# Kernel tuning notes

Measured on AMD Instinct MI355X. Metric: run time of the kernel, lower is better.

The kernel has to match this reference:

```python
import jax, jax.numpy as jnp
import numpy as np
from math import factorial

LMAX = 4
N_COEFF = (LMAX + 1) ** 2      # 25 real spherical-harmonic coefficients
N_RADII = 300                  # distance_bins
N_NODES = 512
FEAT = 128
RES_BETA, RES_ALPHA = 180, 360
DIST_STEP = 0.05


def _sh_basis(lmax, y, alpha):
    """Real spherical harmonics evaluated on a (beta, alpha) product grid.
    y = cos(beta) quadrature nodes. Returns [res_beta, res_alpha, (lmax+1)^2]."""
    B, A = len(y), len(alpha)
    P = np.zeros((lmax + 1, lmax + 1, B))
    P[0, 0] = 1.0
    s = np.sqrt(np.clip(1.0 - y * y, 0.0, None))
    for m in range(1, lmax + 1):
        P[m, m] = -(2 * m - 1) * s * P[m - 1, m - 1]
    for m in range(lmax):
        P[m + 1, m] = (2 * m + 1) * y * P[m, m]
    for m in range(lmax + 1):
        for l in range(m + 2, lmax + 1):
            P[l, m] = ((2 * l - 1) * y * P[l - 1, m] - (l + m - 1) * P[l - 2, m]) / (l - m)
    cols = []
    for l in range(lmax + 1):
        for m in range(-l, l + 1):
            am = abs(m)
            Nlm = np.sqrt((2 * l + 1) / (4 * np.pi) * factorial(l - am) / factorial(l + am))
            if m == 0:
                col = Nlm * P[l, 0][:, None] * np.ones((1, A))
            elif m > 0:
                col = np.sqrt(2.0) * Nlm * P[l, m][:, None] * np.cos(m * alpha)[None, :]
            else:
                col = np.sqrt(2.0) * Nlm * P[l, am][:, None] * np.sin(am * alpha)[None, :]
            cols.append(col)
    return np.stack(cols, axis=-1).astype(np.float32)


def setup_inputs() -> dict:
    key = jax.random.key(0)
    ks = jax.random.split(key, 14)

    def lin(k, a, b):
        return jax.random.normal(k, (a, b), jnp.float32) / np.float32(np.sqrt(a))

    x = jax.random.normal(ks[0], (N_NODES, FEAT), jnp.float32)
    fd = [FEAT, 128, 128, 64, 16, 2]
    td = [FEAT, 128, 128, 128, 128, 128, 6]
    fW = [lin(ks[1 + i], fd[i], fd[i + 1]) for i in range(5)]
    tW = [lin(ks[6 + i], td[i], td[i + 1]) for i in range(6)]
    pos_w = lin(ks[12], 2 * FEAT, N_RADII * N_COEFF)
    type_emb = jax.random.normal(ks[13], (5, FEAT), jnp.float32)

    y_np, w_np = np.polynomial.legendre.leggauss(RES_BETA)
    alpha_np = np.linspace(0.0, 2.0 * np.pi, RES_ALPHA, endpoint=False)
    basis = jnp.asarray(_sh_basis(LMAX, y_np, alpha_np))          # [B, A, C]
    qw = jnp.asarray(w_np / 2.0, jnp.float32)                     # gausslegendre / 2
    y_grid = jnp.asarray(y_np, jnp.float32)
    alpha_grid = jnp.asarray(alpha_np, jnp.float32)

    return {
        "x": x,
        "focus_w1": fW[0], "focus_w2": fW[1], "focus_w3": fW[2], "focus_w4": fW[3], "focus_w5": fW[4],
        "type_w1": tW[0], "type_w2": tW[1], "type_w3": tW[2], "type_w4": tW[3], "type_w5": tW[4], "type_w6": tW[5],
        "pos_w": pos_w, "type_emb": type_emb,
        "basis": basis, "qw": qw, "y_grid": y_grid, "alpha_grid": alpha_grid,
        "res_beta": RES_BETA, "res_alpha": RES_ALPHA,
    }


def reference(x, focus_w1, focus_w2, focus_w3, focus_w4, focus_w5,
              type_w1, type_w2, type_w3, type_w4, type_w5, type_w6,
              pos_w, type_emb, basis, qw, y_grid, alpha_grid,
              res_beta, res_alpha):
    n_nodes = x.shape[0]

    # --- focus MLP (relu), per-node logits; STOP logit 0 appended ---
    h = x
    for W in (focus_w1, focus_w2, focus_w3, focus_w4):
        h = jax.nn.relu(h @ W)
    focus_scores = (h @ focus_w5)[:, 0]                             # [n_nodes]
    focus_probs = jax.nn.softmax(jnp.concatenate([focus_scores, jnp.zeros((1,), x.dtype)]))
    focus = jnp.minimum(jnp.argmax(focus_probs), n_nodes - 1)

    # --- type MLP (softplus) on the focus node's features ---
    feat_f = x[focus]                                               # [128]
    th = feat_f
    for W in (type_w1, type_w2, type_w3, type_w4, type_w5):
        th = jax.nn.softplus(th @ W)
    type_dist = jax.nn.softmax(th @ type_w6)                        # [6]
    type_idx = jnp.minimum(jnp.argmax(type_dist), 4)

    # --- position head: SH coefficients per radial shell ---
    pos_in = jnp.concatenate([feat_f, type_emb[type_idx]])          # [256]
    coeffs = (pos_in @ pos_w).reshape(N_RADII, N_COEFF)             # [R, C]

    # to_s2grid: log-density on the sphere for every radial shell
    f = jnp.einsum('rc,bac->rba', coeffs, basis)                    # [R, B, A]
    log_meas = jnp.log(qw)[:, None] + jnp.log(2.0 * jnp.pi / res_alpha)  # [B, 1]

    # radial distribution: integral of exp(f) over the sphere, per shell
    log_radial = jax.nn.logsumexp(f + log_meas[None], axis=(1, 2))  # [R]
    radial_probs = jax.nn.softmax(log_radial)

    key = jax.random.key(42)
    k_r, k_a = jax.random.split(key)
    r_idx = jax.random.categorical(k_r, log_radial)

    # angular distribution at the sampled radius, normalized on S2
    fr = f[r_idx]                                                   # [B, A]
    logZr = jax.nn.logsumexp(fr + log_meas)
    angular_dist = jnp.exp(fr - logZr)                              # [B, A]

    joint_log = (fr + log_meas - logZr).reshape(-1)
    idx = jax.random.categorical(k_a, joint_log)
    y_i = idx // res_alpha
    a_i = idx % res_alpha

    radius_pred = (r_idx.astype(jnp.float32) + 1.0) * DIST_STEP
    return (type_dist, radial_probs, angular_dist, radius_pred, y_grid[y_i], alpha_grid[a_i])
```

## Files before the change

kernel.cpp:

```cpp
#include <hip/hip_runtime.h>
#include <math.h>
#include <stdint.h>

#define NNODES 512
#define FEAT   128
#define NR     300
#define NC     25
#define NB     180
#define NA     360
#define RSPLIT 4
#define BCHUNK (NB / RSPLIT)
#define O_TYPE   0
#define O_RAD    6
#define O_ANG    306
#define O_RADIUS 65106
#define O_Y      65107
#define O_ALPHA  65108

#define WS_KEYS   0
#define WS_FOCUS  4
#define WS_TYPEI  5
#define WS_RIDX   6
#define WS_INVZ   7
#define WS_DEAD   8
#define WS_SCORES 320
#define WS_POSIN  832
#define WS_PSUM   1088
#define WS_PV     1280
#define WS_PI     1472
#define WS_Q      1664
#define WS_HR     6176
#define WS_COEF   8352
#define WS_LRP    15872

#define GB_MLP   NNODES
#define GB_PREP  36
#define GB_PFT   162
#define GB_PFP   768
#define GB_TOTAL (GB_MLP + GB_PREP + GB_PFT + GB_PFP)

__constant__ int c_m_of_c[25] = {0,-1,0,1,-2,-1,0,1,2,-3,-2,-1,0,1,2,3,-4,-3,-2,-1,0,1,2,3,4};
__constant__ int c_h_cnt[9] = {5,4,3,2,1,4,3,2,1};
__constant__ int c_h_idx[9][5] = {
  {0,2,6,12,20},
  {3,7,13,21,0},
  {8,14,22,0,0},
  {15,23,0,0,0},
  {24,0,0,0,0},
  {1,5,11,19,0},
  {4,10,18,0,0},
  {9,17,0,0,0},
  {16,0,0,0,0}};

__device__ __forceinline__ void tf2x32(uint32_t k0, uint32_t k1, uint32_t x0, uint32_t x1,
                                       uint32_t& o0, uint32_t& o1) {
  uint32_t ks2 = k0 ^ k1 ^ 0x1BD11BDAu;
#define TF_RND(r) { x0 += x1; x1 = (x1 << r) | (x1 >> (32 - r)); x1 ^= x0; }
  x0 += k0; x1 += k1;
  TF_RND(13) TF_RND(15) TF_RND(26) TF_RND(6)
  x0 += k1; x1 += ks2 + 1u;
  TF_RND(17) TF_RND(29) TF_RND(16) TF_RND(24)
  x0 += ks2; x1 += k0 + 2u;
  TF_RND(13) TF_RND(15) TF_RND(26) TF_RND(6)
  x0 += k0; x1 += k1 + 3u;
  TF_RND(17) TF_RND(29) TF_RND(16) TF_RND(24)
  x0 += k1; x1 += ks2 + 4u;
  TF_RND(13) TF_RND(15) TF_RND(26) TF_RND(6)
  x0 += ks2; x1 += k0 + 5u;
#undef TF_RND
  o0 = x0; o1 = x1;
}

__device__ __forceinline__ float gumbel32(uint32_t k0, uint32_t k1, uint32_t lo) {
  uint32_t o0, o1; tf2x32(k0, k1, 0u, lo, o0, o1);
  uint32_t bits = o0 ^ o1;
  float u = __uint_as_float((bits >> 9) | 0x3f800000u) - 1.0f;
  u = fmaxf(u, 1.1754944e-38f);
  return -logf(-logf(u));
}

__global__ __launch_bounds__(128) void k_front(const float* __restrict__ x,
    const float* __restrict__ w1, const float* __restrict__ w2, const float* __restrict__ w3,
    const float* __restrict__ w4, const float* __restrict__ w5,
    const float* __restrict__ basis, const float* __restrict__ alpha_grid,
    const float* __restrict__ tw1, const float* __restrict__ tw2, const float* __restrict__ tw3,
    const float* __restrict__ tw4, const float* __restrict__ tw5, const float* __restrict__ tw6,
    const float* __restrict__ pos_w,
    float* __restrict__ wsf) {
  int bx = blockIdx.x;
  if (bx >= GB_MLP + GB_PREP + GB_PFT) {
    int pb = bx - (GB_MLP + GB_PREP + GB_PFT);
    const float4* p4 = (const float4*)pos_w;
    const int n4 = NR * NC * 256 / 4;
    float acc = 0.f;
    for (int i = pb * 128 + threadIdx.x; i < n4; i += GB_PFP * 128) {
      float4 v = p4[i];
      acc += v.x + v.y + v.z + v.w;
    }
    if (acc == -1.2345678e30f) wsf[WS_DEAD] = acc;
    return;
  }
  if (bx >= GB_MLP + GB_PREP) {
    int pb = bx - (GB_MLP + GB_PREP);
    int base = pb * 128;
    float acc = 0.f;
    int i = base + threadIdx.x;
    const float4* mats[5] = {(const float4*)tw1, (const float4*)tw2, (const float4*)tw3,
                             (const float4*)tw4, (const float4*)tw5};
    int mi = pb >> 5;
    if (mi < 5) {
      int li = (pb & 31) * 128 + threadIdx.x;
      float4 v = mats[mi][li];
      acc += v.x + v.y + v.z + v.w;
    } else {
      int li = (pb - 160) * 128 + threadIdx.x;
      if (li < 192) { float4 v = ((const float4*)tw6)[li]; acc += v.x + v.y + v.z + v.w; }
    }
    (void)i;
    if (acc == -1.2345678e30f) wsf[WS_DEAD] = acc;
    return;
  }
  if (bx >= GB_MLP) {
    int t = (bx - GB_MLP) * 128 + threadIdx.x;
    if (bx == GB_MLP && threadIdx.x == 0) {
      uint32_t* wu = (uint32_t*)wsf;
      uint32_t o0, o1;
      tf2x32(0u, 42u, 0u, 0u, o0, o1); wu[WS_KEYS + 0] = o0; wu[WS_KEYS + 1] = o1;
      tf2x32(0u, 42u, 0u, 1u, o0, o1); wu[WS_KEYS + 2] = o0; wu[WS_KEYS + 3] = o1;
    }
    if (t < NB * NC) {
      int b = t / NC, c = t % NC;
      int m = c_m_of_c[c];
      float q;
      if (m >= 0) {
        q = basis[(b * NA + 0) * NC + c];
      } else {
        float a10 = alpha_grid[10];
        q = basis[(b * NA + 10) * NC + c] / sinf((float)(-m) * a10);
      }
      wsf[WS_Q + t] = q;
    }
    return;
  }
  __shared__ float ha[128], hb[128];
  int n = bx, j = threadIdx.x;
  ha[j] = x[n * FEAT + j];
  __syncthreads();
  float acc = 0.f;
#pragma unroll 8
  for (int k = 0; k < 128; k++) acc += ha[k] * w1[k * 128 + j];
  hb[j] = fmaxf(acc, 0.f);
  __syncthreads();
  acc = 0.f;
#pragma unroll 8
  for (int k = 0; k < 128; k++) acc += hb[k] * w2[k * 128 + j];
  ha[j] = fmaxf(acc, 0.f);
  __syncthreads();
  if (j < 64) {
    acc = 0.f;
#pragma unroll 8
    for (int k = 0; k < 128; k++) acc += ha[k] * w3[k * 64 + j];
    hb[j] = fmaxf(acc, 0.f);
  }
  __syncthreads();
  if (j < 16) {
    acc = 0.f;
#pragma unroll
    for (int k = 0; k < 64; k++) acc += hb[k] * w4[k * 16 + j];
    ha[j] = fmaxf(acc, 0.f);
  }
  __syncthreads();
  if (j == 0) {
    acc = 0.f;
#pragma unroll
    for (int k = 0; k < 16; k++) acc += ha[k] * w5[k * 2 + 0];
    wsf[WS_SCORES + n] = acc;
  }
}

__global__ __launch_bounds__(1024) void k_type(const float* __restrict__ x,
    const float* __restrict__ w1, const float* __restrict__ w2, const float* __restrict__ w3,
    const float* __restrict__ w4, const float* __restrict__ w5, const float* __restrict__ w6,
    const float* __restrict__ type_emb, float* __restrict__ out, float* __restrict__ wsf) {
  __shared__ float src[128];
  __shared__ float partial[8][128];
  __shared__ float wrv[16]; __shared__ int wri[16];
  __shared__ float lg[6];
  __shared__ int f_sh, ti_sh;
  int t = threadIdx.x;
  int lane = t & 63, wid = t >> 6;
  float bv = -INFINITY; int bi = 1 << 30;
  if (t < NNODES + 1) { bv = (t < NNODES) ? wsf[WS_SCORES + t] : 0.f; bi = t; }
  for (int off = 32; off; off >>= 1) {
    float v2 = __shfl_down(bv, off); int i2 = __shfl_down(bi, off);
    if (v2 > bv || (v2 == bv && i2 < bi)) { bv = v2; bi = i2; }
  }
  if (lane == 0) { wrv[wid] = bv; wri[wid] = bi; }
  __syncthreads();
  if (t == 0) {
    float v0 = wrv[0]; int i0 = wri[0];
    for (int w = 1; w < 16; w++)
      if (wrv[w] > v0 || (wrv[w] == v0 && wri[w] < i0)) { v0 = wrv[w]; i0 = wri[w]; }
    int focus = (i0 < NNODES - 1) ? i0 : (NNODES - 1);
    ((int*)wsf)[WS_FOCUS] = focus;
    f_sh = focus;
  }
  __syncthreads();
  int focus = f_sh;
  if (t < 128) { float xv = x[focus * FEAT + t]; src[t] = xv; wsf[WS_POSIN + t] = xv; }
  __syncthreads();
  const float* Ws[5] = {w1, w2, w3, w4, w5};
#pragma unroll
  for (int L = 0; L < 5; L++) {
    const float* W = Ws[L];
    int j = t & 127, kc = t >> 7;
    float acc = 0.f;
#pragma unroll
    for (int k = 0; k < 16; k++) acc += src[kc * 16 + k] * W[(kc * 16 + k) * 128 + j];
    partial[kc][j] = acc;
    __syncthreads();
    if (t < 128) {
      float s = 0.f;
#pragma unroll
      for (int q = 0; q < 8; q++) s += partial[q][t];
      src[t] = fmaxf(s, 0.f) + log1pf(expf(-fabsf(s)));
    }
    __syncthreads();
  }
  float prod = 0.f;
  if (t < 768) { int o = t >> 7, j = t & 127; prod = src[j] * w6[j * 6 + o]; }
  for (int off = 32; off; off >>= 1) prod += __shfl_down(prod, off);
  if (t < 768 && lane == 0) wrv[wid] = prod;
  __syncthreads();
  if (t == 0) {
    for (int o = 0; o < 6; o++) lg[o] = wrv[2 * o] + wrv[2 * o + 1];
    float M = lg[0]; int am = 0;
    for (int i = 1; i < 6; i++) if (lg[i] > M) { M = lg[i]; am = i; }
    float e[6], S = 0.f;
    for (int i = 0; i < 6; i++) { e[i] = expf(lg[i] - M); S += e[i]; }
    for (int i = 0; i < 6; i++) out[O_TYPE + i] = e[i] / S;
    int ti = (am < 4) ? am : 4;
    ((int*)wsf)[WS_TYPEI] = ti;
    ti_sh = ti;
  }
  __syncthreads();
  if (t < 128) wsf[WS_POSIN + 128 + t] = type_emb[ti_sh * FEAT + t];
}

__global__ __launch_bounds__(256) void k_coeffs(const float* __restrict__ pos_w,
                                                float* __restrict__ wsf) {
  __shared__ float pin[256];
  __shared__ float partial[4][64];
  int t = threadIdx.x;
  pin[t] = wsf[WS_POSIN + t];
  __syncthreads();
  int oL = t & 63, kc = t >> 6;
  int o = blockIdx.x * 64 + oL;
  float acc = 0.f;
  if (o < NR * NC) {
#pragma unroll 16
    for (int k = 0; k < 64; k++) acc += pin[kc * 64 + k] * pos_w[(kc * 64 + k) * (NR * NC) + o];
  }
  partial[kc][oL] = acc;
  __syncthreads();
  if (kc == 0 && o < NR * NC)
    wsf[WS_COEF + o] = partial[0][oL] + partial[1][oL] + partial[2][oL] + partial[3][oL];
}

__global__ __launch_bounds__(384) void k_radial_lse(const float* __restrict__ qw,
    const float* __restrict__ alpha_grid, float* __restrict__ wsf) {
  __shared__ float4 Hs4[BCHUNK * 3];
  __shared__ float cs[NC];
  __shared__ float wred[6];
  int bx = blockIdx.x;
  int r = bx >> 2, s = bx & 3;
  int b0 = s * BCHUNK;
  int t = threadIdx.x;
  float* Hs = (float*)Hs4;
  if (t < NC) cs[t] = wsf[WS_COEF + r * NC + t];
  __syncthreads();
  const float LOGM = -4.0482054576f;
  for (int p = t; p < BCHUNK * 9; p += 384) {
    int b = p / 9, jj = p % 9;
    int bg = b0 + b;
    int n = c_h_cnt[jj];
    float acc = 0.f;
    for (int q = 0; q < n; q++) { int c = c_h_idx[jj][q]; acc += cs[c] * wsf[WS_Q + bg * NC + c]; }
    if (jj == 0) acc += logf(qw[bg]) + LOGM;
    Hs[b * 12 + jj] = acc;
  }
  __syncthreads();
  int a = t;
  float c1 = 0, c2 = 0, c3 = 0, c4 = 0, s1 = 0, s2 = 0, s3 = 0, s4 = 0;
  bool act = a < NA;
  if (act) {
    float al = alpha_grid[a];
    sincosf(al, &s1, &c1);
    sincosf(2.f * al, &s2, &c2);
    sincosf(3.f * al, &s3, &c3);
    sincosf(4.f * al, &s4, &c4);
  }
  float acc = 0.f;
#pragma unroll 5
  for (int b = 0; b < BCHUNK; b++) {
    float4 h0 = Hs4[b * 3 + 0], h1 = Hs4[b * 3 + 1], h2 = Hs4[b * 3 + 2];
    float f = h0.x + h0.y * c1 + h0.z * c2 + h0.w * c3 + h1.x * c4
            + h1.y * s1 + h1.z * s2 + h1.w * s3 + h2.x * s4;
    acc += act ? __expf(f) : 0.f;
  }
  for (int off = 32; off; off >>= 1) acc += __shfl_down(acc, off);
  int wid = t >> 6, lane = t & 63;
  if (lane == 0) wred[wid] = acc;
  __syncthreads();
  if (t == 0) {
    float ss = 0.f;
    for (int w = 0; w < 6; w++) ss += wred[w];
    wsf[WS_LRP + bx] = ss;
  }
}

__global__ __launch_bounds__(256) void k_radial_sample(float* __restrict__ out,
                                                       float* __restrict__ wsf) {
  __shared__ float ssh[NR], lrsh[NR];
  __shared__ float wr[4]; __shared__ int wi[4];
  __shared__ float Ssh; __shared__ int rsh;
  int t = threadIdx.x;
  const uint32_t* wu = (const uint32_t*)wsf;
  uint32_t kr0 = wu[WS_KEYS + 0], kr1 = wu[WS_KEYS + 1];
  for (int i = t; i < NR; i += 256) {
    float s = wsf[WS_LRP + i * 4] + wsf[WS_LRP + i * 4 + 1]
            + wsf[WS_LRP + i * 4 + 2] + wsf[WS_LRP + i * 4 + 3];
    ssh[i] = s;
    lrsh[i] = logf(s);
  }
  __syncthreads();
  float ss = 0.f;
  for (int i = t; i < NR; i += 256) ss += ssh[i];
  for (int off = 32; off; off >>= 1) ss += __shfl_down(ss, off);
  if ((t & 63) == 0) wr[t >> 6] = ss;
  __syncthreads();
  if (t == 0) Ssh = wr[0] + wr[1] + wr[2] + wr[3];
  __syncthreads();
  float S = Ssh;
  for (int i = t; i < NR; i += 256) out[O_RAD + i] = ssh[i] / S;
  float bv = -INFINITY; int bi = 1 << 30;
  for (int i = t; i < NR; i += 256) {
    float v = lrsh[i] + gumbel32(kr0, kr1, (uint32_t)i);
    if (v > bv || (v == bv && i < bi)) { bv = v; bi = i; }
  }
  for (int off = 32; off; off >>= 1) {
    float v2 = __shfl_down(bv, off); int i2 = __shfl_down(bi, off);
    if (v2 > bv || (v2 == bv && i2 < bi)) { bv = v2; bi = i2; }
  }
  if ((t & 63) == 0) { wr[t >> 6] = bv; wi[t >> 6] = bi; }
  __syncthreads();
  if (t == 0) {
    float v0 = wr[0]; int i0 = wi[0];
    for (int w = 1; w < 4; w++)
      if (wr[w] > v0 || (wr[w] == v0 && wi[w] < i0)) { v0 = wr[w]; i0 = wi[w]; }
    rsh = i0;
    ((int*)wsf)[WS_RIDX] = i0;
    out[O_RADIUS] = (float)(i0 + 1) * 0.05f;
  }
  __syncthreads();
  int r = rsh;
  for (int p = t; p < NB * 9; p += 256) {
    int b = p / 9, jj = p % 9, n = c_h_cnt[jj];
    float acc = 0.f;
    for (int q = 0; q < n; q++) {
      int c = c_h_idx[jj][q];
      acc += wsf[WS_COEF + r * NC + c] * wsf[WS_Q + b * NC + c];
    }
    wsf[WS_HR + b * 12 + jj] = acc;
  }
}

__global__ __launch_bounds__(384) void k_ang_partial(const float* __restrict__ qw,
    const float* __restrict__ alpha_grid, float* __restrict__ out, float* __restrict__ wsf) {
  __shared__ float wred[6]; __shared__ float wrv[6]; __shared__ int wri[6];
  int b = blockIdx.x, t = threadIdx.x;
  const uint32_t* wu = (const uint32_t*)wsf;
  uint32_t ka0 = wu[WS_KEYS + 2], ka1 = wu[WS_KEYS + 3];
  const float4* hr4 = (const float4*)(wsf + WS_HR + b * 12);
  float4 h0 = hr4[0], h1 = hr4[1], h2 = hr4[2];
  const float MEAS = 0.01745329252f;
  float elm = qw[b] * MEAS;
  float lm = logf(elm);
  float e = 0.f, v = -INFINITY; int idx = b * NA + t;
  if (t < NA) {
    float al = alpha_grid[t];
    float s1, c1, s2, c2, s3, c3, s4, c4;
    sincosf(al, &s1, &c1); sincosf(2.f * al, &s2, &c2);
    sincosf(3.f * al, &s3, &c3); sincosf(4.f * al, &s4, &c4);
    float f = h0.x + h0.y * c1 + h0.z * c2 + h0.w * c3 + h1.x * c4
            + h1.y * s1 + h1.z * s2 + h1.w * s3 + h2.x * s4;
    float ef = __expf(f);
    out[O_ANG + idx] = ef;
    e = ef * elm;
    v = f + lm + gumbel32(ka0, ka1, (uint32_t)idx);
  }
  int wid = t >> 6, lane = t & 63;
  for (int off = 32; off; off >>= 1) e += __shfl_down(e, off);
  if (lane == 0) wred[wid] = e;
  for (int off = 32; off; off >>= 1) {
    float v2 = __shfl_down(v, off); int i2 = __shfl_down(idx, off);
    if (v2 > v || (v2 == v && i2 < idx)) { v = v2; idx = i2; }
  }
  if (lane == 0) { wrv[wid] = v; wri[wid] = idx; }
  __syncthreads();
  if (t == 0) {
    float zs = 0.f;
    float v0 = wrv[0]; int i0 = wri[0];
    for (int w = 0; w < 6; w++) {
      zs += wred[w];
      if (w && (wrv[w] > v0 || (wrv[w] == v0 && wri[w] < i0))) { v0 = wrv[w]; i0 = wri[w]; }
    }
    wsf[WS_PSUM + b] = zs;
    wsf[WS_PV + b] = v0;
    ((int*)wsf)[WS_PI + b] = i0;
  }
}

__global__ __launch_bounds__(256) void k_ang_final(const float* __restrict__ y_grid,
    const float* __restrict__ alpha_grid, float* __restrict__ out, float* __restrict__ wsf) {
  __shared__ float wr[4]; __shared__ int wi[4];
  int t = threadIdx.x;
  float sv = (t < NB) ? wsf[WS_PSUM + t] : 0.f;
  for (int off = 32; off; off >>= 1) sv += __shfl_down(sv, off);
  if ((t & 63) == 0) wr[t >> 6] = sv;
  __syncthreads();
  if (t == 0) wsf[WS_INVZ] = 1.0f / (wr[0] + wr[1] + wr[2] + wr[3]);
  __syncthreads();
  float v = (t < NB) ? wsf[WS_PV + t] : -INFINITY;
  int i = (t < NB) ? ((const int*)wsf)[WS_PI + t] : (1 << 30);
  for (int off = 32; off; off >>= 1) {
    float v2 = __shfl_down(v, off); int i2 = __shfl_down(i, off);
    if (v2 > v || (v2 == v && i2 < i)) { v = v2; i = i2; }
  }
  if ((t & 63) == 0) { wr[t >> 6] = v; wi[t >> 6] = i; }
  __syncthreads();
  if (t == 0) {
    float v0 = wr[0]; int i0 = wi[0];
    for (int w = 1; w < 4; w++)
      if (wr[w] > v0 || (wr[w] == v0 && wi[w] < i0)) { v0 = wr[w]; i0 = wi[w]; }
    int yi = i0 / NA, ai = i0 % NA;
    out[O_Y] = y_grid[yi];
    out[O_ALPHA] = alpha_grid[ai];
  }
}

__global__ __launch_bounds__(256) void k_ang_scale(float* __restrict__ out,
                                                   const float* __restrict__ wsf) {
  int i = blockIdx.x * 256 + threadIdx.x;
  float invZ = wsf[WS_INVZ];
  if (i < NB * NA) out[O_ANG + i] *= invZ;
}

extern "C" void kernel_launch(void* const* d_in, const int* in_sizes, int n_in,
                              void* d_out, int out_size, void* d_ws, size_t ws_size,
                              hipStream_t stream) {
  const float* x          = (const float*)d_in[0];
  const float* fw1        = (const float*)d_in[1];
  const float* fw2        = (const float*)d_in[2];
  const float* fw3        = (const float*)d_in[3];
  const float* fw4        = (const float*)d_in[4];
  const float* fw5        = (const float*)d_in[5];
  const float* tw1        = (const float*)d_in[6];
  const float* tw2        = (const float*)d_in[7];
  const float* tw3        = (const float*)d_in[8];
  const float* tw4        = (const float*)d_in[9];
  const float* tw5        = (const float*)d_in[10];
  const float* tw6        = (const float*)d_in[11];
  const float* pos_w      = (const float*)d_in[12];
  const float* type_emb   = (const float*)d_in[13];
  const float* basis      = (const float*)d_in[14];
  const float* qw         = (const float*)d_in[15];
  const float* y_grid     = (const float*)d_in[16];
  const float* alpha_grid = (const float*)d_in[17];
  (void)in_sizes; (void)n_in; (void)out_size; (void)ws_size;
  float* out = (float*)d_out;
  float* wsf = (float*)d_ws;

  k_front<<<GB_TOTAL, 128, 0, stream>>>(x, fw1, fw2, fw3, fw4, fw5, basis, alpha_grid,
                                        tw1, tw2, tw3, tw4, tw5, tw6, pos_w, wsf);
  k_type<<<1, 1024, 0, stream>>>(x, tw1, tw2, tw3, tw4, tw5, tw6, type_emb, out, wsf);
  k_coeffs<<<(NR * NC + 63) / 64, 256, 0, stream>>>(pos_w, wsf);
  k_radial_lse<<<NR * RSPLIT, 384, 0, stream>>>(qw, alpha_grid, wsf);
  k_radial_sample<<<1, 256, 0, stream>>>(out, wsf);
  k_ang_partial<<<NB, 384, 0, stream>>>(qw, alpha_grid, out, wsf);
  k_ang_final<<<1, 256, 0, stream>>>(y_grid, alpha_grid, out, wsf);
  k_ang_scale<<<(NB * NA + 255) / 256, 256, 0, stream>>>(out, wsf);
}
```

Baseline: 65.84 us.

## Reuse radial shell sums for angular normalizer, drop scale kernel, batch MLP nodes

The angular normalizer is now taken from the per-shell exp-sum already computed for the radial distribution (fss[r]), so k_ang_partial writes normalized densities directly. This removes the partial-sum reduction, the k_ang_final sum pass and the whole k_ang_scale launch with its extra read-modify-write of the 64800-entry output. Separately, the front MLP processes 8 nodes per 256-thread block so each weight load is reused across four rows, and the prefetch and prep blocks are consolidated into far fewer, larger blocks. The radial sample kernel is reshaped to 384 threads with one element per thread. The risk is a small numerical difference, since the normalizer now comes from the radial pass rather than a fresh sum over the same shell.

```diff
diff --git a/kernel.cpp b/kernel.cpp
--- a/kernel.cpp
+++ b/kernel.cpp
@@ -25,7 +25,6 @@
 #define WS_DEAD   8
 #define WS_SCORES 320
 #define WS_POSIN  832
-#define WS_PSUM   1088
 #define WS_PV     1280
 #define WS_PI     1472
 #define WS_Q      1664
@@ -33,11 +32,11 @@
 #define WS_COEF   8352
 #define WS_LRP    15872
 
-#define GB_MLP   NNODES
-#define GB_PREP  36
-#define GB_PFT   162
-#define GB_PFP   768
-#define GB_TOTAL (GB_MLP + GB_PREP + GB_PFT + GB_PFP)
+#define G1_MLP   64
+#define G1_PREP  18
+#define G1_PFT   21
+#define G1_PFP   240
+#define G1_TOTAL (G1_MLP + G1_PREP + G1_PFT + G1_PFP)
 
 __constant__ int c_m_of_c[25] = {0,-1,0,1,-2,-1,0,1,2,-3,-2,-1,0,1,2,3,-4,-3,-2,-1,0,1,2,3,4};
 __constant__ int c_h_cnt[9] = {5,4,3,2,1,4,3,2,1};
@@ -79,7 +78,7 @@
   return -logf(-logf(u));
 }
 
-__global__ __launch_bounds__(128) void k_front(const float* __restrict__ x,
+__global__ __launch_bounds__(256) void k_front(const float* __restrict__ x,
     const float* __restrict__ w1, const float* __restrict__ w2, const float* __restrict__ w3,
     const float* __restrict__ w4, const float* __restrict__ w5,
     const float* __restrict__ basis, const float* __restrict__ alpha_grid,
@@ -87,49 +86,79 @@
     const float* __restrict__ tw4, const float* __restrict__ tw5, const float* __restrict__ tw6,
     const float* __restrict__ pos_w,
     float* __restrict__ wsf) {
-  int bx = blockIdx.x;
-  if (bx >= GB_MLP + GB_PREP + GB_PFT) {
-    int pb = bx - (GB_MLP + GB_PREP + GB_PFT);
-    const float4* p4 = (const float4*)pos_w;
-    const int n4 = NR * NC * 256 / 4;
-    float acc = 0.f;
-    for (int i = pb * 128 + threadIdx.x; i < n4; i += GB_PFP * 128) {
-      float4 v = p4[i];
-      acc += v.x + v.y + v.z + v.w;
-    }
-    if (acc == -1.2345678e30f) wsf[WS_DEAD] = acc;
-    return;
-  }
-  if (bx >= GB_MLP + GB_PREP) {
-    int pb = bx - (GB_MLP + GB_PREP);
-    int base = pb * 128;
-    float acc = 0.f;
-    int i = base + threadIdx.x;
-    const float4* mats[5] = {(const float4*)tw1, (const float4*)tw2, (const float4*)tw3,
-                             (const float4*)tw4, (const float4*)tw5};
-    int mi = pb >> 5;
-    if (mi < 5) {
-      int li = (pb & 31) * 128 + threadIdx.x;
-      float4 v = mats[mi][li];
-      acc += v.x + v.y + v.z + v.w;
-    } else {
-      int li = (pb - 160) * 128 + threadIdx.x;
-      if (li < 192) { float4 v = ((const float4*)tw6)[li]; acc += v.x + v.y + v.z + v.w; }
-    }
-    (void)i;
-    if (acc == -1.2345678e30f) wsf[WS_DEAD] = acc;
-    return;
-  }
-  if (bx >= GB_MLP) {
-    int t = (bx - GB_MLP) * 128 + threadIdx.x;
-    if (bx == GB_MLP && threadIdx.x == 0) {
+  __shared__ float A[8][128];
+  __shared__ float B[8][128];
+  int bx = blockIdx.x, t = threadIdx.x;
+
+  if (bx < G1_MLP) {
+    int base = bx * 8;
+    for (int i = t; i < 8 * 128; i += 256) A[i >> 7][i & 127] = x[(base + (i >> 7)) * FEAT + (i & 127)];
+    __syncthreads();
+    int j = t & 127, h = t >> 7;
+    {
+      float a0 = 0, a1 = 0, a2 = 0, a3 = 0;
+#pragma unroll 8
+      for (int k = 0; k < 128; k++) {
+        float wv = w1[k * 128 + j];
+        a0 += A[h * 4 + 0][k] * wv; a1 += A[h * 4 + 1][k] * wv;
+        a2 += A[h * 4 + 2][k] * wv; a3 += A[h * 4 + 3][k] * wv;
+      }
+      __syncthreads();
+      B[h * 4 + 0][j] = fmaxf(a0, 0.f); B[h * 4 + 1][j] = fmaxf(a1, 0.f);
+      B[h * 4 + 2][j] = fmaxf(a2, 0.f); B[h * 4 + 3][j] = fmaxf(a3, 0.f);
+      __syncthreads();
+    }
+    {
+      float a0 = 0, a1 = 0, a2 = 0, a3 = 0;
+#pragma unroll 8
+      for (int k = 0; k < 128; k++) {
+        float wv = w2[k * 128 + j];
+        a0 += B[h * 4 + 0][k] * wv; a1 += B[h * 4 + 1][k] * wv;
+        a2 += B[h * 4 + 2][k] * wv; a3 += B[h * 4 + 3][k] * wv;
+      }
+      __syncthreads();
+      A[h * 4 + 0][j] = fmaxf(a0, 0.f); A[h * 4 + 1][j] = fmaxf(a1, 0.f);
+      A[h * 4 + 2][j] = fmaxf(a2, 0.f); A[h * 4 + 3][j] = fmaxf(a3, 0.f);
+      __syncthreads();
+    }
+    {
+      int j3 = t & 63, g = t >> 6;
+      float a0 = 0, a1 = 0;
+#pragma unroll 8
+      for (int k = 0; k < 128; k++) {
+        float wv = w3[k * 64 + j3];
+        a0 += A[g * 2 + 0][k] * wv; a1 += A[g * 2 + 1][k] * wv;
+      }
+      __syncthreads();
+      B[g * 2 + 0][j3] = fmaxf(a0, 0.f); B[g * 2 + 1][j3] = fmaxf(a1, 0.f);
+      __syncthreads();
+    }
+    {
+      int j4 = t & 15, g4 = t >> 4;
+      if (g4 < 8) {
+        float a0 = 0;
+#pragma unroll
+        for (int k = 0; k < 64; k++) a0 += B[g4][k] * w4[k * 16 + j4];
+        A[g4][j4] = fmaxf(a0, 0.f);
+      }
+      __syncthreads();
+    }
+    if (t < 8) {
+      float a0 = 0;
+#pragma unroll
+      for (int k = 0; k < 16; k++) a0 += A[t][k] * w5[k * 2 + 0];
+      wsf[WS_SCORES + base + t] = a0;
+    }
+  } else if (bx < G1_MLP + G1_PREP) {
+    int p = (bx - G1_MLP) * 256 + t;
+    if (bx == G1_MLP && t == 0) {
       uint32_t* wu = (uint32_t*)wsf;
       uint32_t o0, o1;
       tf2x32(0u, 42u, 0u, 0u, o0, o1); wu[WS_KEYS + 0] = o0; wu[WS_KEYS + 1] = o1;
       tf2x32(0u, 42u, 0u, 1u, o0, o1); wu[WS_KEYS + 2] = o0; wu[WS_KEYS + 3] = o1;
     }
-    if (t < NB * NC) {
-      int b = t / NC, c = t % NC;
+    if (p < NB * NC) {
+      int b = p / NC, c = p % NC;
       int m = c_m_of_c[c];
       float q;
       if (m >= 0) {
@@ -138,43 +167,30 @@
         float a10 = alpha_grid[10];
         q = basis[(b * NA + 10) * NC + c] / sinf((float)(-m) * a10);
       }
-      wsf[WS_Q + t] = q;
-    }
-    return;
-  }
-  __shared__ float ha[128], hb[128];
-  int n = bx, j = threadIdx.x;
-  ha[j] = x[n * FEAT + j];
-  __syncthreads();
-  float acc = 0.f;
-#pragma unroll 8
-  for (int k = 0; k < 128; k++) acc += ha[k] * w1[k * 128 + j];
-  hb[j] = fmaxf(acc, 0.f);
-  __syncthreads();
-  acc = 0.f;
-#pragma unroll 8
-  for (int k = 0; k < 128; k++) acc += hb[k] * w2[k * 128 + j];
-  ha[j] = fmaxf(acc, 0.f);
-  __syncthreads();
-  if (j < 64) {
-    acc = 0.f;
-#pragma unroll 8
-    for (int k = 0; k < 128; k++) acc += ha[k] * w3[k * 64 + j];
-    hb[j] = fmaxf(acc, 0.f);
-  }
-  __syncthreads();
-  if (j < 16) {
-    acc = 0.f;
-#pragma unroll
-    for (int k = 0; k < 64; k++) acc += hb[k] * w4[k * 16 + j];
-    ha[j] = fmaxf(acc, 0.f);
-  }
-  __syncthreads();
-  if (j == 0) {
-    acc = 0.f;
-#pragma unroll
-    for (int k = 0; k < 16; k++) acc += ha[k] * w5[k * 2 + 0];
-    wsf[WS_SCORES + n] = acc;
+      wsf[WS_Q + p] = q;
+    }
+  } else if (bx < G1_MLP + G1_PREP + G1_PFT) {
+    const float4* mats[5] = {(const float4*)tw1, (const float4*)tw2, (const float4*)tw3,
+                             (const float4*)tw4, (const float4*)tw5};
+    int lid = (bx - (G1_MLP + G1_PREP)) * 256 + t;
+    float acc = 0.f;
+    for (int vi = lid; vi < 20672; vi += G1_PFT * 256) {
+      int mi = vi >> 12;
+      float4 v;
+      if (mi < 5) v = mats[mi][vi & 4095];
+      else        v = ((const float4*)tw6)[vi - 20480];
+      acc += v.x + v.y + v.z + v.w;
+    }
+    if (acc == -1.2345678e30f) wsf[WS_DEAD] = acc;
+  } else {
+    int lid = (bx - (G1_MLP + G1_PREP + G1_PFT)) * 256 + t;
+    const float4* p4 = (const float4*)pos_w;
+    float acc = 0.f;
+    for (int i = lid; i < NR * NC * 256 / 4; i += G1_PFP * 256) {
+      float4 v = p4[i];
+      acc += v.x + v.y + v.z + v.w;
+    }
+    if (acc == -1.2345678e30f) wsf[WS_DEAD] = acc;
   }
 }
 
@@ -290,11 +306,10 @@
     Hs[b * 12 + jj] = acc;
   }
   __syncthreads();
-  int a = t;
   float c1 = 0, c2 = 0, c3 = 0, c4 = 0, s1 = 0, s2 = 0, s3 = 0, s4 = 0;
-  bool act = a < NA;
+  bool act = t < NA;
   if (act) {
-    float al = alpha_grid[a];
+    float al = alpha_grid[t];
     sincosf(al, &s1, &c1);
     sincosf(2.f * al, &s2, &c2);
     sincosf(3.f * al, &s3, &c3);
@@ -319,52 +334,53 @@
   }
 }
 
-__global__ __launch_bounds__(256) void k_radial_sample(float* __restrict__ out,
+__global__ __launch_bounds__(384) void k_radial_sample(float* __restrict__ out,
                                                        float* __restrict__ wsf) {
-  __shared__ float ssh[NR], lrsh[NR];
-  __shared__ float wr[4]; __shared__ int wi[4];
-  __shared__ float Ssh; __shared__ int rsh;
-  int t = threadIdx.x;
+  __shared__ float wred[6]; __shared__ int wri[6];
+  __shared__ float fss[NR];
+  __shared__ float S_sh; __shared__ int r_sh;
+  int t = threadIdx.x, lane = t & 63, wid = t >> 6;
   const uint32_t* wu = (const uint32_t*)wsf;
   uint32_t kr0 = wu[WS_KEYS + 0], kr1 = wu[WS_KEYS + 1];
-  for (int i = t; i < NR; i += 256) {
-    float s = wsf[WS_LRP + i * 4] + wsf[WS_LRP + i * 4 + 1]
-            + wsf[WS_LRP + i * 4 + 2] + wsf[WS_LRP + i * 4 + 3];
-    ssh[i] = s;
-    lrsh[i] = logf(s);
-  }
-  __syncthreads();
-  float ss = 0.f;
-  for (int i = t; i < NR; i += 256) ss += ssh[i];
+  float sv = 0.f, lr = -INFINITY;
+  if (t < NR) {
+    sv = wsf[WS_LRP + 4 * t] + wsf[WS_LRP + 4 * t + 1]
+       + wsf[WS_LRP + 4 * t + 2] + wsf[WS_LRP + 4 * t + 3];
+    fss[t] = sv;
+    lr = logf(sv);
+  }
+  float ss = sv;
   for (int off = 32; off; off >>= 1) ss += __shfl_down(ss, off);
-  if ((t & 63) == 0) wr[t >> 6] = ss;
-  __syncthreads();
-  if (t == 0) Ssh = wr[0] + wr[1] + wr[2] + wr[3];
-  __syncthreads();
-  float S = Ssh;
-  for (int i = t; i < NR; i += 256) out[O_RAD + i] = ssh[i] / S;
-  float bv = -INFINITY; int bi = 1 << 30;
-  for (int i = t; i < NR; i += 256) {
-    float v = lrsh[i] + gumbel32(kr0, kr1, (uint32_t)i);
-    if (v > bv || (v == bv && i < bi)) { bv = v; bi = i; }
-  }
+  if (lane == 0) wred[wid] = ss;
+  __syncthreads();
+  if (t == 0) {
+    float S = 0.f;
+    for (int w = 0; w < 6; w++) S += wred[w];
+    S_sh = S;
+  }
+  __syncthreads();
+  if (t < NR) out[O_RAD + t] = sv / S_sh;
+  float v = (t < NR) ? lr + gumbel32(kr0, kr1, (uint32_t)t) : -INFINITY;
+  int bi = (t < NR) ? t : (1 << 30);
   for (int off = 32; off; off >>= 1) {
-    float v2 = __shfl_down(bv, off); int i2 = __shfl_down(bi, off);
-    if (v2 > bv || (v2 == bv && i2 < bi)) { bv = v2; bi = i2; }
-  }
-  if ((t & 63) == 0) { wr[t >> 6] = bv; wi[t >> 6] = bi; }
-  __syncthreads();
-  if (t == 0) {
-    float v0 = wr[0]; int i0 = wi[0];
-    for (int w = 1; w < 4; w++)
-      if (wr[w] > v0 || (wr[w] == v0 && wi[w] < i0)) { v0 = wr[w]; i0 = wi[w]; }
-    rsh = i0;
+    float v2 = __shfl_down(v, off); int i2 = __shfl_down(bi, off);
+    if (v2 > v || (v2 == v && i2 < bi)) { v = v2; bi = i2; }
+  }
+  __syncthreads();
+  if (lane == 0) { wred[wid] = v; wri[wid] = bi; }
+  __syncthreads();
+  if (t == 0) {
+    float v0 = wred[0]; int i0 = wri[0];
+    for (int w = 1; w < 6; w++)
+      if (wred[w] > v0 || (wred[w] == v0 && wri[w] < i0)) { v0 = wred[w]; i0 = wri[w]; }
+    r_sh = i0;
     ((int*)wsf)[WS_RIDX] = i0;
     out[O_RADIUS] = (float)(i0 + 1) * 0.05f;
-  }
-  __syncthreads();
-  int r = rsh;
-  for (int p = t; p < NB * 9; p += 256) {
+    wsf[WS_INVZ] = 1.0f / fss[i0];
+  }
+  __syncthreads();
+  int r = r_sh;
+  for (int p = t; p < NB * 9; p += 384) {
     int b = p / 9, jj = p % 9, n = c_h_cnt[jj];
     float acc = 0.f;
     for (int q = 0; q < n; q++) {
@@ -377,8 +393,9 @@
 
 __global__ __launch_bounds__(384) void k_ang_partial(const float* __restrict__ qw,
     const float* __restrict__ alpha_grid, float* __restrict__ out, float* __restrict__ wsf) {
-  __shared__ float wred[6]; __shared__ float wrv[6]; __shared__ int wri[6];
+  __shared__ float wrv[6]; __shared__ int wri[6];
   int b = blockIdx.x, t = threadIdx.x;
+  int lane = t & 63, wid = t >> 6;
   const uint32_t* wu = (const uint32_t*)wsf;
   uint32_t ka0 = wu[WS_KEYS + 2], ka1 = wu[WS_KEYS + 3];
   const float4* hr4 = (const float4*)(wsf + WS_HR + b * 12);
@@ -386,7 +403,8 @@
   const float MEAS = 0.01745329252f;
   float elm = qw[b] * MEAS;
   float lm = logf(elm);
-  float e = 0.f, v = -INFINITY; int idx = b * NA + t;
+  float invZ = wsf[WS_INVZ];
+  float v = -INFINITY; int idx = (t < NA) ? b * NA + t : (1 << 30);
   if (t < NA) {
     float al = alpha_grid[t];
     float s1, c1, s2, c2, s3, c3, s4, c4;
@@ -394,14 +412,9 @@
     sincosf(3.f * al, &s3, &c3); sincosf(4.f * al, &s4, &c4);
     float f = h0.x + h0.y * c1 + h0.z * c2 + h0.w * c3 + h1.x * c4
             + h1.y * s1 + h1.z * s2 + h1.w * s3 + h2.x * s4;
-    float ef = __expf(f);
-    out[O_ANG + idx] = ef;
-    e = ef * elm;
+    out[O_ANG + idx] = __expf(f) * invZ;
     v = f + lm + gumbel32(ka0, ka1, (uint32_t)idx);
   }
-  int wid = t >> 6, lane = t & 63;
-  for (int off = 32; off; off >>= 1) e += __shfl_down(e, off);
-  if (lane == 0) wred[wid] = e;
   for (int off = 32; off; off >>= 1) {
     float v2 = __shfl_down(v, off); int i2 = __shfl_down(idx, off);
     if (v2 > v || (v2 == v && i2 < idx)) { v = v2; idx = i2; }
@@ -409,13 +422,9 @@
   if (lane == 0) { wrv[wid] = v; wri[wid] = idx; }
   __syncthreads();
   if (t == 0) {
-    float zs = 0.f;
     float v0 = wrv[0]; int i0 = wri[0];
-    for (int w = 0; w < 6; w++) {
-      zs += wred[w];
-      if (w && (wrv[w] > v0 || (wrv[w] == v0 && wri[w] < i0))) { v0 = wrv[w]; i0 = wri[w]; }
-    }
-    wsf[WS_PSUM + b] = zs;
+    for (int w = 1; w < 6; w++)
+      if (wrv[w] > v0 || (wrv[w] == v0 && wri[w] < i0)) { v0 = wrv[w]; i0 = wri[w]; }
     wsf[WS_PV + b] = v0;
     ((int*)wsf)[WS_PI + b] = i0;
   }
@@ -424,20 +433,14 @@
 __global__ __launch_bounds__(256) void k_ang_final(const float* __restrict__ y_grid,
     const float* __restrict__ alpha_grid, float* __restrict__ out, float* __restrict__ wsf) {
   __shared__ float wr[4]; __shared__ int wi[4];
-  int t = threadIdx.x;
-  float sv = (t < NB) ? wsf[WS_PSUM + t] : 0.f;
-  for (int off = 32; off; off >>= 1) sv += __shfl_down(sv, off);
-  if ((t & 63) == 0) wr[t >> 6] = sv;
-  __syncthreads();
-  if (t == 0) wsf[WS_INVZ] = 1.0f / (wr[0] + wr[1] + wr[2] + wr[3]);
-  __syncthreads();
+  int t = threadIdx.x, lane = t & 63, wid = t >> 6;
   float v = (t < NB) ? wsf[WS_PV + t] : -INFINITY;
   int i = (t < NB) ? ((const int*)wsf)[WS_PI + t] : (1 << 30);
   for (int off = 32; off; off >>= 1) {
     float v2 = __shfl_down(v, off); int i2 = __shfl_down(i, off);
     if (v2 > v || (v2 == v && i2 < i)) { v = v2; i = i2; }
   }
-  if ((t & 63) == 0) { wr[t >> 6] = v; wi[t >> 6] = i; }
+  if (lane == 0) { wr[wid] = v; wi[wid] = i; }
   __syncthreads();
   if (t == 0) {
     float v0 = wr[0]; int i0 = wi[0];
@@ -447,13 +450,6 @@
     out[O_Y] = y_grid[yi];
     out[O_ALPHA] = alpha_grid[ai];
   }
-}
-
-__global__ __launch_bounds__(256) void k_ang_scale(float* __restrict__ out,
-                                                   const float* __restrict__ wsf) {
-  int i = blockIdx.x * 256 + threadIdx.x;
-  float invZ = wsf[WS_INVZ];
-  if (i < NB * NA) out[O_ANG + i] *= invZ;
 }
 
 extern "C" void kernel_launch(void* const* d_in, const int* in_sizes, int n_in,
@@ -481,13 +477,12 @@
   float* out = (float*)d_out;
   float* wsf = (float*)d_ws;
 
-  k_front<<<GB_TOTAL, 128, 0, stream>>>(x, fw1, fw2, fw3, fw4, fw5, basis, alpha_grid,
+  k_front<<<G1_TOTAL, 256, 0, stream>>>(x, fw1, fw2, fw3, fw4, fw5, basis, alpha_grid,
                                         tw1, tw2, tw3, tw4, tw5, tw6, pos_w, wsf);
   k_type<<<1, 1024, 0, stream>>>(x, tw1, tw2, tw3, tw4, tw5, tw6, type_emb, out, wsf);
   k_coeffs<<<(NR * NC + 63) / 64, 256, 0, stream>>>(pos_w, wsf);
   k_radial_lse<<<NR * RSPLIT, 384, 0, stream>>>(qw, alpha_grid, wsf);
-  k_radial_sample<<<1, 256, 0, stream>>>(out, wsf);
+  k_radial_sample<<<1, 384, 0, stream>>>(out, wsf);
   k_ang_partial<<<NB, 384, 0, stream>>>(qw, alpha_grid, out, wsf);
   k_ang_final<<<1, 256, 0, stream>>>(y_grid, alpha_grid, out, wsf);
-  k_ang_scale<<<(NB * NA + 255) / 256, 256, 0, stream>>>(out, wsf);
-}
+}
```

Measured after the change: 63.79 us. -3.1%, faster.
